# Kernel tuning notes

Hardware: AMD Instinct MI355X
Metric: run time of the kernel (lower is better)

The kernel has to match this reference:

```python
import jax, jax.numpy as jnp
import numpy as np

N_NODES = 100000
N_EDGES = 1200000
IN_DIM, HIDDEN, OUT_DIM = 128, 64, 64


def setup_inputs() -> dict:
    key = jax.random.key(0)
    k1, k2, k3, k4 = jax.random.split(key, 4)
    x = jax.random.normal(k1, (N_NODES, IN_DIM), dtype=jnp.float32)
    edge_index = jax.random.randint(k2, (2, N_EDGES), 0, N_NODES, dtype=jnp.int64)
    # Glorot-style init for GCNConv linear weights (PyG uses glorot), zero bias.
    W1 = jax.random.normal(k3, (IN_DIM, HIDDEN), dtype=jnp.float32) * np.float32(np.sqrt(2.0 / (IN_DIM + HIDDEN)))
    b1 = jnp.zeros((HIDDEN,), dtype=jnp.float32)
    W2 = jax.random.normal(k4, (HIDDEN, OUT_DIM), dtype=jnp.float32) * np.float32(np.sqrt(2.0 / (HIDDEN + OUT_DIM)))
    b2 = jnp.zeros((OUT_DIM,), dtype=jnp.float32)
    return {"x": x, "edge_index": edge_index, "W1": W1, "b1": b1, "W2": W2, "b2": b2}


def _gcn_conv(h, src, dst, deg_inv_sqrt, W, b):
    # PyG GCNConv: out = scatter_add( norm * (h @ W)[src] -> dst ) + b
    n = h.shape[0]
    norm = deg_inv_sqrt[src] * deg_inv_sqrt[dst]            # [E+N]
    hw = h @ W                                              # [N, F_out]
    msg = hw[src] * norm[:, None]                           # [E+N, F_out] gather
    out = jnp.zeros((n, W.shape[1]), h.dtype).at[dst].add(msg)  # scatter-add
    return out + b


def reference(x, edge_index, W1, b1, W2, b2):
    n = x.shape[0]
    # Add self-loops (GCNConv default add_self_loops=True).
    loop = jnp.arange(n, dtype=edge_index.dtype)
    src = jnp.concatenate([edge_index[0], loop])  # source nodes
    dst = jnp.concatenate([edge_index[1], loop])  # target nodes (aggregation)
    # Symmetric normalization D^{-1/2} (A+I) D^{-1/2}; degree at targets.
    deg = jnp.zeros((n,), x.dtype).at[dst].add(jnp.ones((), x.dtype))
    deg_inv_sqrt = jnp.where(deg > 0, jax.lax.rsqrt(deg), 0.0)
    h = _gcn_conv(x, src, dst, deg_inv_sqrt, W1, b1)
    h = jax.nn.relu(h)
    h = _gcn_conv(h, src, dst, deg_inv_sqrt, W2, b2)
    h = jax.nn.relu(h)
    return h
```

## Files before the change

kernel.cpp:

```cpp
#include <hip/hip_runtime.h>
#include <hip/hip_fp16.h>
#include <cstdint>
#include <cstddef>

#define NN 100000
#define NE 1200000
#define NBKT 1563
#define CAP_B 1536
#define PBLK 128
#define PCHK ((NE + PBLK - 1) / PBLK)

typedef _Float16 f16x8 __attribute__((ext_vector_type(8)));
typedef float f32x4 __attribute__((ext_vector_type(4)));

__global__ void zero_kernel(int* __restrict__ cur, unsigned* __restrict__ ovfn) {
    int i = blockIdx.x * blockDim.x + threadIdx.x;
    if (i < NBKT) cur[i] = 0;
    if (i == NBKT) *ovfn = 0;
}

__global__ __launch_bounds__(256) void partition_hier(
    const int* __restrict__ ei, int* __restrict__ cur,
    unsigned* __restrict__ recs, unsigned* __restrict__ ovfn,
    uint2* __restrict__ ovf, int E) {
    __shared__ int hist[NBKT];
    __shared__ int base[NBKT];
    const int tid = threadIdx.x;
    for (int i = tid; i < NBKT; i += 256) hist[i] = 0;
    __syncthreads();
    const int lo = blockIdx.x * PCHK, hi = min(lo + PCHK, E);
    for (int e = lo + tid; e < hi; e += 256)
        atomicAdd(&hist[ei[E + e] >> 6], 1);
    __syncthreads();
    for (int i = tid; i < NBKT; i += 256) {
        int c = hist[i];
        base[i] = c ? atomicAdd(&cur[i], c) : 0;
        hist[i] = 0;
    }
    __syncthreads();
    for (int e = lo + tid; e < hi; e += 256) {
        int d = ei[E + e];
        int s = ei[e];
        int b = d >> 6;
        int lp = atomicAdd(&hist[b], 1);
        int pos = base[b] + lp;
        if (pos < CAP_B)
            recs[(size_t)b * CAP_B + pos] = ((unsigned)s << 6) | (unsigned)(d & 63);
        else {
            unsigned o = atomicAdd(ovfn, 1);
            if (o < 4096) ovf[o] = make_uint2((unsigned)s, (unsigned)d);
        }
    }
}

__global__ __launch_bounds__(256) void bucket_dis(
    const int* __restrict__ cur, const unsigned* __restrict__ recs,
    const unsigned* __restrict__ ovfn, const uint2* __restrict__ ovf,
    float* __restrict__ dis, int n) {
    __shared__ int cnt[64];
    const int b = blockIdx.x, tid = threadIdx.x;
    if (tid < 64) cnt[tid] = 0;
    __syncthreads();
    int c = min(cur[b], CAP_B);
    const unsigned* st = recs + (size_t)b * CAP_B;
    for (int i = tid; i < c; i += 256) atomicAdd(&cnt[st[i] & 63], 1);
    __syncthreads();
    if (tid < 64) {
        int g = b * 64 + tid;
        if (g < n) {
            int cc = cnt[tid];
            unsigned no = *ovfn;
            for (unsigned i = 0; i < no; i++)
                if ((int)ovf[i].y == g) cc++;
            dis[g] = rsqrtf((float)cc + 1.0f);
        }
    }
}

template <bool HALF_OUT>
__global__ __launch_bounds__(256) void agg_bucket3(
    const int* __restrict__ cur, const unsigned* __restrict__ recs,
    const __half* __restrict__ hw, const float* __restrict__ dis,
    const float* __restrict__ bias, void* __restrict__ outv,
    const unsigned* __restrict__ ovfn, const uint2* __restrict__ ovf, int n) {
    __shared__ unsigned srec[CAP_B];
    __shared__ int cnt[64], off[65], woff[64], pfx[64];
    __shared__ float disD[64];
    const int b = blockIdx.x, tid = threadIdx.x;
    if (tid < 64) {
        cnt[tid] = 0;
        int g = b * 64 + tid;
        disD[tid] = (g < n) ? dis[g] : 0.f;
    }
    __syncthreads();

    const int c = min(cur[b], CAP_B);
    const unsigned* st = recs + (size_t)b * CAP_B;
    for (int i = tid; i < c; i += 256) atomicAdd(&cnt[st[i] & 63], 1);
    __syncthreads();
    if (tid < 64) pfx[tid] = cnt[tid];
    __syncthreads();
    for (int s = 1; s < 64; s <<= 1) {
        int v = (tid < 64 && tid >= s) ? pfx[tid - s] : 0;
        __syncthreads();
        if (tid < 64) pfx[tid] += v;
        __syncthreads();
    }
    if (tid == 0) off[0] = 0;
    if (tid < 64) { off[tid + 1] = pfx[tid]; woff[tid] = pfx[tid] - cnt[tid]; }
    __syncthreads();
    for (int i = tid; i < c; i += 256) {
        unsigned k = st[i];
        int p = atomicAdd(&woff[k & 63], 1);
        srec[p] = k;
    }
    __syncthreads();

    const uint2* hwq = (const uint2*)hw;
    const int slot = tid >> 4, sub = tid & 15;
    const unsigned no = *ovfn;
    const float4 bb = ((const float4*)bias)[sub];

#define LD1(q) { float2 g01 = __half22float2(*(__half2*)&(q).x); \
                 float2 g23 = __half22float2(*(__half2*)&(q).y); \
                 a0 += g01.x; a1 += g01.y; a2 += g23.x; a3 += g23.y; }

    for (int j = 0; j < 4; j++) {
        int nl = slot * 4 + j;
        int g = b * 64 + nl;
        if (g >= n) break;
        uint2 qs = hwq[(size_t)g * 16 + sub];
        float a0 = 0.f, a1 = 0.f, a2 = 0.f, a3 = 0.f;
        LD1(qs);

        int e = off[nl], end = off[nl + 1];
        for (; e + 8 <= end; e += 8) {
            uint2 q0 = hwq[(size_t)(srec[e + 0] >> 6) * 16 + sub];
            uint2 q1 = hwq[(size_t)(srec[e + 1] >> 6) * 16 + sub];
            uint2 q2 = hwq[(size_t)(srec[e + 2] >> 6) * 16 + sub];
            uint2 q3 = hwq[(size_t)(srec[e + 3] >> 6) * 16 + sub];
            uint2 q4 = hwq[(size_t)(srec[e + 4] >> 6) * 16 + sub];
            uint2 q5 = hwq[(size_t)(srec[e + 5] >> 6) * 16 + sub];
            uint2 q6 = hwq[(size_t)(srec[e + 6] >> 6) * 16 + sub];
            uint2 q7 = hwq[(size_t)(srec[e + 7] >> 6) * 16 + sub];
            LD1(q0); LD1(q1); LD1(q2); LD1(q3);
            LD1(q4); LD1(q5); LD1(q6); LD1(q7);
        }
        for (; e + 4 <= end; e += 4) {
            uint2 q0 = hwq[(size_t)(srec[e + 0] >> 6) * 16 + sub];
            uint2 q1 = hwq[(size_t)(srec[e + 1] >> 6) * 16 + sub];
            uint2 q2 = hwq[(size_t)(srec[e + 2] >> 6) * 16 + sub];
            uint2 q3 = hwq[(size_t)(srec[e + 3] >> 6) * 16 + sub];
            LD1(q0); LD1(q1); LD1(q2); LD1(q3);
        }
        for (; e < end; e++) {
            uint2 q = hwq[(size_t)(srec[e] >> 6) * 16 + sub];
            LD1(q);
        }
        for (unsigned i = 0; i < no; i++) {
            uint2 o = ovf[i];
            if ((int)o.y == g) { uint2 q = hwq[(size_t)o.x * 16 + sub]; LD1(q); }
        }
        float di = disD[nl];
        float o0 = fmaf(di, a0, bb.x);
        float o1 = fmaf(di, a1, bb.y);
        float o2 = fmaf(di, a2, bb.z);
        float o3 = fmaf(di, a3, bb.w);
        o0 = o0 > 0.f ? o0 : 0.f;
        o1 = o1 > 0.f ? o1 : 0.f;
        o2 = o2 > 0.f ? o2 : 0.f;
        o3 = o3 > 0.f ? o3 : 0.f;
        if (HALF_OUT) {
            __half2 p01 = __floats2half2_rn(o0, o1);
            __half2 p23 = __floats2half2_rn(o2, o3);
            uint2 pk;
            pk.x = *(unsigned*)&p01;
            pk.y = *(unsigned*)&p23;
            ((uint2*)outv)[(size_t)g * 16 + sub] = pk;
        } else {
            float4 oo; oo.x = o0; oo.y = o1; oo.z = o2; oo.w = o3;
            ((float4*)outv)[(size_t)g * 16 + sub] = oo;
        }
    }
#undef LD1
}

template <int K>
__global__ __launch_bounds__(256) void gemm_mfma(const float* __restrict__ A,
                                                 const float* __restrict__ W,
                                                 const float* __restrict__ dis,
                                                 __half* __restrict__ C, int n) {
    constexpr int KB = K / 32;
    __shared__ f16x8 sAf[4 * KB * 64];
    __shared__ f16x8 sWf[4 * KB * 64];
    __shared__ float sdis[64];
    const int tid = threadIdx.x;
    const int row0 = blockIdx.x * 64;

    if (tid < 64) {
        int rw = row0 + tid;
        sdis[tid] = (rw < n) ? dis[rw] : 0.f;
    }

    _Float16* sAh = (_Float16*)sAf;
    const float4* A4 = (const float4*)A;
#pragma unroll
    for (int it = 0; it < K / 16; ++it) {
        int f = it * 256 + tid;
        int row = f / (K / 4);
        int kq = f % (K / 4);
        int k0 = kq * 4;
        float4 a;
        if (row0 + row < n) a = A4[(size_t)(row0 + row) * (K / 4) + kq];
        else { a.x = 0.f; a.y = 0.f; a.z = 0.f; a.w = 0.f; }
        int rt = row >> 4;
        int kb = k0 >> 5;
        int lane = (row & 15) | (((k0 >> 3) & 3) << 4);
        int base = ((rt * KB + kb) * 64 + lane) * 8 + (k0 & 7);
        sAh[base + 0] = (_Float16)a.x;
        sAh[base + 1] = (_Float16)a.y;
        sAh[base + 2] = (_Float16)a.z;
        sAh[base + 3] = (_Float16)a.w;
    }
    _Float16* sWh = (_Float16*)sWf;
    {
        int nn = tid & 63;
        int ct = nn >> 4;
        int lbase = nn & 15;
        for (int k = tid >> 6; k < K; k += 4) {
            float w = W[(size_t)k * 64 + nn];
            int kb = k >> 5;
            int lane = lbase | (((k >> 3) & 3) << 4);
            sWh[((ct * KB + kb) * 64 + lane) * 8 + (k & 7)] = (_Float16)w;
        }
    }
    __syncthreads();

    const int wv = tid >> 6;
    const int lane = tid & 63;
    f32x4 acc[4];
#pragma unroll
    for (int rt = 0; rt < 4; ++rt) acc[rt] = (f32x4){0.f, 0.f, 0.f, 0.f};

#pragma unroll
    for (int kb = 0; kb < KB; ++kb) {
        f16x8 bf = sWf[(wv * KB + kb) * 64 + lane];
#pragma unroll
        for (int rt = 0; rt < 4; ++rt) {
            f16x8 af = sAf[(rt * KB + kb) * 64 + lane];
            acc[rt] = __builtin_amdgcn_mfma_f32_16x16x32_f16(af, bf, acc[rt], 0, 0, 0);
        }
    }

    int col = wv * 16 + (lane & 15);
    int rbase = (lane >> 4) * 4;
#pragma unroll
    for (int rt = 0; rt < 4; ++rt) {
#pragma unroll
        for (int r = 0; r < 4; ++r) {
            int row = row0 + rt * 16 + rbase + r;
            if (row < n)
                C[(size_t)row * 64 + col] = __float2half(acc[rt][r] * sdis[rt * 16 + rbase + r]);
        }
    }
}

__global__ __launch_bounds__(256) void gemm_mfma_h(const __half* __restrict__ A,
                                                   const float* __restrict__ W,
                                                   const float* __restrict__ dis,
                                                   __half* __restrict__ C, int n) {
    constexpr int K = 64, KB = 2;
    __shared__ f16x8 sAf[4 * KB * 64];
    __shared__ f16x8 sWf[4 * KB * 64];
    __shared__ float sdis[64];
    const int tid = threadIdx.x;
    const int row0 = blockIdx.x * 64;

    if (tid < 64) {
        int rw = row0 + tid;
        sdis[tid] = (rw < n) ? dis[rw] : 0.f;
    }

    _Float16* sAh = (_Float16*)sAf;
    const uint2* A2 = (const uint2*)A;
#pragma unroll
    for (int it = 0; it < 4; ++it) {
        int f = it * 256 + tid;
        int row = f >> 4;
        int kq = f & 15;
        int k0 = kq * 4;
        uint2 a;
        if (row0 + row < n) a = A2[(size_t)(row0 + row) * 16 + kq];
        else { a.x = 0u; a.y = 0u; }
        _Float16* ap = (_Float16*)&a;
        int rt = row >> 4;
        int kb = k0 >> 5;
        int lane = (row & 15) | (((k0 >> 3) & 3) << 4);
        int base = ((rt * KB + kb) * 64 + lane) * 8 + (k0 & 7);
        sAh[base + 0] = ap[0];
        sAh[base + 1] = ap[1];
        sAh[base + 2] = ap[2];
        sAh[base + 3] = ap[3];
    }
    _Float16* sWh = (_Float16*)sWf;
    {
        int nn = tid & 63;
        int ct = nn >> 4;
        int lbase = nn & 15;
        for (int k = tid >> 6; k < K; k += 4) {
            float w = W[(size_t)k * 64 + nn];
            int kb = k >> 5;
            int lane = lbase | (((k >> 3) & 3) << 4);
            sWh[((ct * KB + kb) * 64 + lane) * 8 + (k & 7)] = (_Float16)w;
        }
    }
    __syncthreads();

    const int wv = tid >> 6;
    const int lane = tid & 63;
    f32x4 acc[4];
#pragma unroll
    for (int rt = 0; rt < 4; ++rt) acc[rt] = (f32x4){0.f, 0.f, 0.f, 0.f};

#pragma unroll
    for (int kb = 0; kb < KB; ++kb) {
        f16x8 bf = sWf[(wv * KB + kb) * 64 + lane];
#pragma unroll
        for (int rt = 0; rt < 4; ++rt) {
            f16x8 af = sAf[(rt * KB + kb) * 64 + lane];
            acc[rt] = __builtin_amdgcn_mfma_f32_16x16x32_f16(af, bf, acc[rt], 0, 0, 0);
        }
    }

    int col = wv * 16 + (lane & 15);
    int rbase = (lane >> 4) * 4;
#pragma unroll
    for (int rt = 0; rt < 4; ++rt) {
#pragma unroll
        for (int r = 0; r < 4; ++r) {
            int row = row0 + rt * 16 + rbase + r;
            if (row < n)
                C[(size_t)row * 64 + col] = __float2half(acc[rt][r] * sdis[rt * 16 + rbase + r]);
        }
    }
}

__global__ void fill_kernel(float* __restrict__ p, float v, int n) {
    int i = blockIdx.x * blockDim.x + threadIdx.x;
    if (i < n) p[i] = v;
}
__global__ void degree_kernel(const int* __restrict__ ei, float* __restrict__ deg, int E) {
    int stride = gridDim.x * blockDim.x;
    for (int e = blockIdx.x * blockDim.x + threadIdx.x; e < E; e += stride)
        atomicAdd(&deg[ei[E + e]], 1.0f);
}
__global__ void rsqrt_kernel(float* __restrict__ deg, int n) {
    int i = blockIdx.x * blockDim.x + threadIdx.x;
    if (i < n) deg[i] = rsqrtf(deg[i]);
}
template <int K>
__global__ __launch_bounds__(256) void gemm_tile(const float* __restrict__ A,
                                                 const float* __restrict__ W,
                                                 float* __restrict__ C, int n) {
    __shared__ float sA[64 * K];
    __shared__ float sW[K * 64];
    const int tid = threadIdx.x;
    const int row0 = blockIdx.x * 64;
    const int rows = min(64, n - row0);
    const float4* W4 = (const float4*)W;
    float4* sW4 = (float4*)sW;
    for (int i = tid; i < K * 16; i += 256) sW4[i] = W4[i];
    const float4* A4 = (const float4*)(A + (size_t)row0 * K);
    float4* sA4 = (float4*)sA;
    const int nElem = rows * (K / 4);
    for (int i = tid; i < nElem; i += 256) sA4[i] = A4[i];
    __syncthreads();
    const int col = tid & 63;
    const int ty  = tid >> 6;
    float acc[16];
#pragma unroll
    for (int r = 0; r < 16; r++) acc[r] = 0.f;
    for (int k = 0; k < K; k += 4) {
        float w0 = sW[(k + 0) * 64 + col];
        float w1 = sW[(k + 1) * 64 + col];
        float w2 = sW[(k + 2) * 64 + col];
        float w3 = sW[(k + 3) * 64 + col];
#pragma unroll
        for (int r = 0; r < 16; r++) {
            const float4 a = *(const float4*)&sA[(ty + 4 * r) * K + k];
            acc[r] = fmaf(a.x, w0, acc[r]);
            acc[r] = fmaf(a.y, w1, acc[r]);
            acc[r] = fmaf(a.z, w2, acc[r]);
            acc[r] = fmaf(a.w, w3, acc[r]);
        }
    }
#pragma unroll
    for (int r = 0; r < 16; r++) {
        int row = ty + 4 * r;
        if (row < rows) C[(size_t)(row0 + row) * 64 + col] = acc[r];
    }
}
__global__ void scatter_kernel(const int* __restrict__ ei, const float* __restrict__ hw,
                               const float* __restrict__ dis, float* __restrict__ agg, int E) {
    int gtid = blockIdx.x * blockDim.x + threadIdx.x;
    int wave = gtid >> 6, lane = threadIdx.x & 63;
    int nwaves = (gridDim.x * blockDim.x) >> 6;
    for (int e = wave; e < E; e += nwaves) {
        int s = ei[e], d = ei[E + e];
        float v = hw[(size_t)s * 64 + lane] * dis[s] * dis[d];
        atomicAdd(&agg[(size_t)d * 64 + lane], v);
    }
}
__global__ void finalize_kernel(float* __restrict__ agg, const float* __restrict__ hw,
                                const float* __restrict__ dis, const float* __restrict__ b, int n) {
    int i = blockIdx.x * blockDim.x + threadIdx.x;
    if (i < n * 64) {
        int node = i >> 6, col = i & 63;
        float di = dis[node];
        float v = agg[i] + hw[i] * di * di + b[col];
        agg[i] = v > 0.0f ? v : 0.0f;
    }
}

extern "C" void kernel_launch(void* const* d_in, const int* in_sizes, int n_in,
                              void* d_out, int out_size, void* d_ws, size_t ws_size,
                              hipStream_t stream) {
    const float* x  = (const float*)d_in[0];
    const int*   ei = (const int*)d_in[1];
    const float* W1 = (const float*)d_in[2];
    const float* b1 = (const float*)d_in[3];
    const float* W2 = (const float*)d_in[4];
    const float* b2 = (const float*)d_in[5];
    float* out = (float*)d_out;

    const int N = NN, E = NE;
    char* ws = (char*)d_ws;
    const int gemmGrid = (N + 63) / 64;

    if (ws_size >= 38200000u) {
        float*    dis  = (float*)ws;
        int*      cur  = (int*)(ws + (1u << 19));
        unsigned* ovfn = (unsigned*)(ws + 589824u);
        uint2*    ovf  = (uint2*)(ws + 593920u);
        unsigned* recs = (unsigned*)(ws + (1u << 20));
        __half*   hwa  = (__half*)(ws + 11534336u);
        __half*   hvb  = (__half*)(ws + 25165824u);

        zero_kernel<<<(NBKT + 256) / 256, 256, 0, stream>>>(cur, ovfn);
        partition_hier<<<PBLK, 256, 0, stream>>>(ei, cur, recs, ovfn, ovf, E);
        bucket_dis<<<NBKT, 256, 0, stream>>>(cur, recs, ovfn, ovf, dis, N);

        gemm_mfma<128><<<gemmGrid, 256, 0, stream>>>(x, W1, dis, hwa, N);
        agg_bucket3<true><<<NBKT, 256, 0, stream>>>(cur, recs, hwa, dis, b1, hvb, ovfn, ovf, N);
        gemm_mfma_h<<<gemmGrid, 256, 0, stream>>>(hvb, W2, dis, hwa, N);
        agg_bucket3<false><<<NBKT, 256, 0, stream>>>(cur, recs, hwa, dis, b2, out, ovfn, ovf, N);
    } else {
        float* dis  = (float*)ws;
        float* bufA = (float*)(ws + (1 << 19));
        const size_t featBytes = (size_t)N * 64 * sizeof(float);

        fill_kernel<<<(N + 255) / 256, 256, 0, stream>>>(dis, 1.0f, N);
        degree_kernel<<<2048, 256, 0, stream>>>(ei, dis, E);
        rsqrt_kernel<<<(N + 255) / 256, 256, 0, stream>>>(dis, N);

        gemm_tile<128><<<gemmGrid, 256, 0, stream>>>(x, W1, bufA, N);
        hipMemsetAsync(out, 0, featBytes, stream);
        scatter_kernel<<<2048, 256, 0, stream>>>(ei, bufA, dis, out, E);
        finalize_kernel<<<(N * 64 + 255) / 256, 256, 0, stream>>>(out, bufA, dis, b1, N);

        gemm_tile<64><<<gemmGrid, 256, 0, stream>>>(out, W2, bufA, N);
        hipMemsetAsync(out, 0, featBytes, stream);
        scatter_kernel<<<2048, 256, 0, stream>>>(ei, bufA, dis, out, E);
        finalize_kernel<<<(N * 64 + 255) / 256, 256, 0, stream>>>(out, bufA, dis, b2, N);
    }
}
```

Baseline: 130.5 us.

## Sort bucket records once in preprocessing and reuse per-node offsets in both aggregations

The bucket degree kernel now also counting-sorts each bucket's edge records by local destination in shared memory, writes them back as plain source indices, and stores per-node offsets. Both aggregation kernels then load the pre-sorted slab and offsets directly, so the histogram, prefix scan and scatter no longer run twice. The partition kernel's block count is also doubled. The cost is an extra read/write pass over the record slabs in the preprocessing kernel and a new offset array in the workspace.

```diff
diff --git a/kernel.cpp b/kernel.cpp
--- a/kernel.cpp
+++ b/kernel.cpp
@@ -7,7 +7,7 @@
 #define NE 1200000
 #define NBKT 1563
 #define CAP_B 1536
-#define PBLK 128
+#define PBLK 256
 #define PCHK ((NE + PBLK - 1) / PBLK)
 
 typedef _Float16 f16x8 __attribute__((ext_vector_type(8)));
@@ -53,18 +53,37 @@
     }
 }
 
-__global__ __launch_bounds__(256) void bucket_dis(
-    const int* __restrict__ cur, const unsigned* __restrict__ recs,
+__global__ __launch_bounds__(256) void sort_bucket(
+    const int* __restrict__ cur, unsigned* __restrict__ recs,
     const unsigned* __restrict__ ovfn, const uint2* __restrict__ ovf,
-    float* __restrict__ dis, int n) {
-    __shared__ int cnt[64];
+    float* __restrict__ dis, int* __restrict__ offn, int n) {
+    __shared__ unsigned raw[CAP_B], srt[CAP_B];
+    __shared__ int cnt[64], pfx[64], woff[64];
     const int b = blockIdx.x, tid = threadIdx.x;
     if (tid < 64) cnt[tid] = 0;
-    __syncthreads();
-    int c = min(cur[b], CAP_B);
-    const unsigned* st = recs + (size_t)b * CAP_B;
-    for (int i = tid; i < c; i += 256) atomicAdd(&cnt[st[i] & 63], 1);
-    __syncthreads();
+    const int c = min(cur[b], CAP_B);
+    unsigned* slab = recs + (size_t)b * CAP_B;
+    for (int i = tid; i < c; i += 256) raw[i] = slab[i];
+    __syncthreads();
+    for (int i = tid; i < c; i += 256) atomicAdd(&cnt[raw[i] & 63], 1);
+    __syncthreads();
+    if (tid < 64) pfx[tid] = cnt[tid];
+    __syncthreads();
+    for (int s = 1; s < 64; s <<= 1) {
+        int v = (tid < 64 && tid >= s) ? pfx[tid - s] : 0;
+        __syncthreads();
+        if (tid < 64) pfx[tid] += v;
+        __syncthreads();
+    }
+    if (tid < 64) woff[tid] = pfx[tid] - cnt[tid];
+    __syncthreads();
+    for (int i = tid; i < c; i += 256) {
+        unsigned k = raw[i];
+        int p = atomicAdd(&woff[k & 63], 1);
+        srt[p] = k >> 6;
+    }
+    __syncthreads();
+    for (int i = tid; i < c; i += 256) slab[i] = srt[i];
     if (tid < 64) {
         int g = b * 64 + tid;
         if (g < n) {
@@ -73,47 +92,31 @@
             for (unsigned i = 0; i < no; i++)
                 if ((int)ovf[i].y == g) cc++;
             dis[g] = rsqrtf((float)cc + 1.0f);
+            offn[g] = pfx[tid] - cnt[tid];
         }
     }
 }
 
 template <bool HALF_OUT>
-__global__ __launch_bounds__(256) void agg_bucket3(
+__global__ __launch_bounds__(256) void agg_bucket4(
     const int* __restrict__ cur, const unsigned* __restrict__ recs,
-    const __half* __restrict__ hw, const float* __restrict__ dis,
-    const float* __restrict__ bias, void* __restrict__ outv,
+    const int* __restrict__ offn, const __half* __restrict__ hw,
+    const float* __restrict__ dis, const float* __restrict__ bias,
+    void* __restrict__ outv,
     const unsigned* __restrict__ ovfn, const uint2* __restrict__ ovf, int n) {
     __shared__ unsigned srec[CAP_B];
-    __shared__ int cnt[64], off[65], woff[64], pfx[64];
+    __shared__ int soff[65];
     __shared__ float disD[64];
     const int b = blockIdx.x, tid = threadIdx.x;
+    const int c = min(cur[b], CAP_B);
+    const unsigned* slab = recs + (size_t)b * CAP_B;
+    for (int i = tid; i < c; i += 256) srec[i] = slab[i];
     if (tid < 64) {
-        cnt[tid] = 0;
         int g = b * 64 + tid;
         disD[tid] = (g < n) ? dis[g] : 0.f;
-    }
-    __syncthreads();
-
-    const int c = min(cur[b], CAP_B);
-    const unsigned* st = recs + (size_t)b * CAP_B;
-    for (int i = tid; i < c; i += 256) atomicAdd(&cnt[st[i] & 63], 1);
-    __syncthreads();
-    if (tid < 64) pfx[tid] = cnt[tid];
-    __syncthreads();
-    for (int s = 1; s < 64; s <<= 1) {
-        int v = (tid < 64 && tid >= s) ? pfx[tid - s] : 0;
-        __syncthreads();
-        if (tid < 64) pfx[tid] += v;
-        __syncthreads();
-    }
-    if (tid == 0) off[0] = 0;
-    if (tid < 64) { off[tid + 1] = pfx[tid]; woff[tid] = pfx[tid] - cnt[tid]; }
-    __syncthreads();
-    for (int i = tid; i < c; i += 256) {
-        unsigned k = st[i];
-        int p = atomicAdd(&woff[k & 63], 1);
-        srec[p] = k;
-    }
+        soff[tid] = (g < n) ? offn[g] : c;
+    }
+    if (tid == 0) soff[64] = c;
     __syncthreads();
 
     const uint2* hwq = (const uint2*)hw;
@@ -133,28 +136,28 @@
         float a0 = 0.f, a1 = 0.f, a2 = 0.f, a3 = 0.f;
         LD1(qs);
 
-        int e = off[nl], end = off[nl + 1];
+        int e = soff[nl], end = (nl < 63) ? soff[nl + 1] : soff[64];
         for (; e + 8 <= end; e += 8) {
-            uint2 q0 = hwq[(size_t)(srec[e + 0] >> 6) * 16 + sub];
-            uint2 q1 = hwq[(size_t)(srec[e + 1] >> 6) * 16 + sub];
-            uint2 q2 = hwq[(size_t)(srec[e + 2] >> 6) * 16 + sub];
-            uint2 q3 = hwq[(size_t)(srec[e + 3] >> 6) * 16 + sub];
-            uint2 q4 = hwq[(size_t)(srec[e + 4] >> 6) * 16 + sub];
-            uint2 q5 = hwq[(size_t)(srec[e + 5] >> 6) * 16 + sub];
-            uint2 q6 = hwq[(size_t)(srec[e + 6] >> 6) * 16 + sub];
-            uint2 q7 = hwq[(size_t)(srec[e + 7] >> 6) * 16 + sub];
+            uint2 q0 = hwq[(size_t)srec[e + 0] * 16 + sub];
+            uint2 q1 = hwq[(size_t)srec[e + 1] * 16 + sub];
+            uint2 q2 = hwq[(size_t)srec[e + 2] * 16 + sub];
+            uint2 q3 = hwq[(size_t)srec[e + 3] * 16 + sub];
+            uint2 q4 = hwq[(size_t)srec[e + 4] * 16 + sub];
+            uint2 q5 = hwq[(size_t)srec[e + 5] * 16 + sub];
+            uint2 q6 = hwq[(size_t)srec[e + 6] * 16 + sub];
+            uint2 q7 = hwq[(size_t)srec[e + 7] * 16 + sub];
             LD1(q0); LD1(q1); LD1(q2); LD1(q3);
             LD1(q4); LD1(q5); LD1(q6); LD1(q7);
         }
         for (; e + 4 <= end; e += 4) {
-            uint2 q0 = hwq[(size_t)(srec[e + 0] >> 6) * 16 + sub];
-            uint2 q1 = hwq[(size_t)(srec[e + 1] >> 6) * 16 + sub];
-            uint2 q2 = hwq[(size_t)(srec[e + 2] >> 6) * 16 + sub];
-            uint2 q3 = hwq[(size_t)(srec[e + 3] >> 6) * 16 + sub];
+            uint2 q0 = hwq[(size_t)srec[e + 0] * 16 + sub];
+            uint2 q1 = hwq[(size_t)srec[e + 1] * 16 + sub];
+            uint2 q2 = hwq[(size_t)srec[e + 2] * 16 + sub];
+            uint2 q3 = hwq[(size_t)srec[e + 3] * 16 + sub];
             LD1(q0); LD1(q1); LD1(q2); LD1(q3);
         }
         for (; e < end; e++) {
-            uint2 q = hwq[(size_t)(srec[e] >> 6) * 16 + sub];
+            uint2 q = hwq[(size_t)srec[e] * 16 + sub];
             LD1(q);
         }
         for (unsigned i = 0; i < no; i++) {
@@ -442,18 +445,19 @@
         int*      cur  = (int*)(ws + (1u << 19));
         unsigned* ovfn = (unsigned*)(ws + 589824u);
         uint2*    ovf  = (uint2*)(ws + 593920u);
-        unsigned* recs = (unsigned*)(ws + (1u << 20));
+        int*      offn = (int*)(ws + 655360u);
+        unsigned* recs = (unsigned*)(ws + 1572864u);
         __half*   hwa  = (__half*)(ws + 11534336u);
         __half*   hvb  = (__half*)(ws + 25165824u);
 
         zero_kernel<<<(NBKT + 256) / 256, 256, 0, stream>>>(cur, ovfn);
         partition_hier<<<PBLK, 256, 0, stream>>>(ei, cur, recs, ovfn, ovf, E);
-        bucket_dis<<<NBKT, 256, 0, stream>>>(cur, recs, ovfn, ovf, dis, N);
+        sort_bucket<<<NBKT, 256, 0, stream>>>(cur, recs, ovfn, ovf, dis, offn, N);
 
         gemm_mfma<128><<<gemmGrid, 256, 0, stream>>>(x, W1, dis, hwa, N);
-        agg_bucket3<true><<<NBKT, 256, 0, stream>>>(cur, recs, hwa, dis, b1, hvb, ovfn, ovf, N);
+        agg_bucket4<true><<<NBKT, 256, 0, stream>>>(cur, recs, offn, hwa, dis, b1, hvb, ovfn, ovf, N);
         gemm_mfma_h<<<gemmGrid, 256, 0, stream>>>(hvb, W2, dis, hwa, N);
-        agg_bucket3<false><<<NBKT, 256, 0, stream>>>(cur, recs, hwa, dis, b2, out, ovfn, ovf, N);
+        agg_bucket4<false><<<NBKT, 256, 0, stream>>>(cur, recs, offn, hwa, dis, b2, out, ovfn, ovf, N);
     } else {
         float* dis  = (float*)ws;
         float* bufA = (float*)(ws + (1 << 19));
```

After: 123.7 us. -5.2%, faster.
